# Kernel optimization log

Measured on AMD Instinct MI355X. Metric: run time of the kernel, lower is better.

## Reference

```python
import jax, jax.numpy as jnp
import numpy as np

B, N = 16384, 1024


def _bit_reversal_indices(n):
    bits = int(np.log2(n))
    val = np.arange(n)
    src = np.zeros(n, dtype=np.int64)
    for _ in range(bits):
        src = (src << 1) | (val & 1)
        val = val >> 1
    return src  # src[k] = source pair for target pair k


def _inter_stage_indices(n, stage_idx):
    prev = 2 ** stage_idx
    kb = np.arange(n // 2)
    g = kb // prev
    kw = kb % prev
    half = (kw >= prev // 2).astype(np.int64)
    off = kw % (prev // 2)
    nb = prev // 2
    sE = (2 * g) * nb + off
    sO = (2 * g + 1) * nb + off
    perm = np.empty(n, dtype=np.int64)
    perm[2 * kb] = 2 * sE + half
    perm[2 * kb + 1] = 2 * sO + half
    return perm


def _final_unscramble_indices(n):
    k = np.arange(n // 2)
    perm = np.empty(n, dtype=np.int64)
    perm[k] = 2 * k
    perm[k + n // 2] = 2 * k + 1
    return perm


def _butterfly_weights(n, stage_idx):
    # grouped 1x1 conv weights -> (n//2, 4, 4): out = W[g] @ in per group
    Nb = 2 ** (stage_idx + 1)
    nub = Nb // 2
    reps = n // Nb
    k = np.arange(nub)
    rW = np.cos(2.0 * np.pi * k / Nb)      # Re(W_Nb^k)
    iW = -np.sin(2.0 * np.pi * k / Nb)     # Im(W_Nb^k) (forward DFT twiddle)
    W = np.zeros((nub, 4, 4), dtype=np.float32)
    W[:, 0, 0] = 1.0; W[:, 0, 2] = rW;  W[:, 0, 3] = -iW
    W[:, 1, 1] = 1.0; W[:, 1, 2] = iW;  W[:, 1, 3] = rW
    W[:, 2, 0] = 1.0; W[:, 2, 2] = -rW; W[:, 2, 3] = iW
    W[:, 3, 1] = 1.0; W[:, 3, 2] = -iW; W[:, 3, 3] = -rW
    return np.tile(W, (reps, 1, 1))  # (n//2, 4, 4)


def setup_inputs() -> dict:
    key = jax.random.key(0)
    x = jax.random.normal(key, (B, 2 * N, 1, 1), dtype=jnp.float32)
    return {"x": x}


def reference(x) -> jnp.ndarray:
    b = x.shape[0]
    n = x.shape[1] // 2
    stages = int(np.log2(n))
    # pairs view: (B, N, 2) = interleaved [Re, Im]
    v = x.reshape(b, n, 2)
    v = v[:, jnp.asarray(_bit_reversal_indices(n)), :]
    for s in range(stages):
        if s > 0:
            v = v[:, jnp.asarray(_inter_stage_indices(n, s)), :]
        W = jnp.asarray(_butterfly_weights(n, s))       # (N/2, 4, 4)
        g = v.reshape(b, n // 2, 4)                     # 4 channels per group
        g = jnp.einsum('goi,bgi->bgo', W, g)            # grouped 1x1 conv
        v = g.reshape(b, n, 2)
    v = v[:, jnp.asarray(_final_unscramble_indices(n)), :]
    return v.reshape(b, 2 * n, 1, 1)
```

## Files before the change

### kernel.cpp

```cpp
#include <hip/hip_runtime.h>

#define NFFT 1024

__device__ __forceinline__ float2 cmul(float2 a, float2 b) {
  return make_float2(fmaf(a.x, b.x, -a.y * b.y), fmaf(a.x, b.y, a.y * b.x));
}
__device__ __forceinline__ float2 cadd(float2 a, float2 b) { return make_float2(a.x + b.x, a.y + b.y); }
__device__ __forceinline__ float2 csub(float2 a, float2 b) { return make_float2(a.x - b.x, a.y - b.y); }

__device__ __forceinline__ void dft4(const float2 v[4], float2 y[4]) {
  float2 s02 = cadd(v[0], v[2]), d02 = csub(v[0], v[2]);
  float2 s13 = cadd(v[1], v[3]), d13 = csub(v[1], v[3]);
  y[0] = cadd(s02, s13);
  y[2] = csub(s02, s13);
  y[1] = make_float2(d02.x + d13.y, d02.y - d13.x);
  y[3] = make_float2(d02.x - d13.y, d02.y + d13.x);
}

__device__ __forceinline__ int phys(int s) {
  return (s & ~15) | (((s & 15) + (s >> 4)) & 15);
}

__device__ __forceinline__ void dft16_store(float2 v[16], float2* S, int base, int stride) {
  #pragma unroll
  for (int n2 = 0; n2 < 4; ++n2) {
    float2 a[4] = {v[n2], v[n2 + 4], v[n2 + 8], v[n2 + 12]};
    float2 y[4];
    dft4(a, y);
    v[n2] = y[0]; v[n2 + 4] = y[1]; v[n2 + 8] = y[2]; v[n2 + 12] = y[3];
  }
  const float C1 = 0.9238795325112867f;
  const float S1 = 0.3826834323650898f;
  const float R2 = 0.7071067811865476f;
  v[1 + 4]  = cmul(v[1 + 4],  make_float2(C1, -S1));
  v[1 + 8]  = cmul(v[1 + 8],  make_float2(R2, -R2));
  v[1 + 12] = cmul(v[1 + 12], make_float2(S1, -C1));
  v[2 + 4]  = cmul(v[2 + 4],  make_float2(R2, -R2));
  v[2 + 8]  = make_float2(v[2 + 8].y, -v[2 + 8].x);
  v[2 + 12] = cmul(v[2 + 12], make_float2(-R2, -R2));
  v[3 + 4]  = cmul(v[3 + 4],  make_float2(S1, -C1));
  v[3 + 8]  = cmul(v[3 + 8],  make_float2(-R2, -R2));
  v[3 + 12] = cmul(v[3 + 12], make_float2(-C1, S1));
  #pragma unroll
  for (int k1 = 0; k1 < 4; ++k1) {
    float2 a[4] = {v[4 * k1], v[4 * k1 + 1], v[4 * k1 + 2], v[4 * k1 + 3]};
    float2 y[4];
    dft4(a, y);
    #pragma unroll
    for (int k2 = 0; k2 < 4; ++k2) {
      int k = k1 + 4 * k2;
      S[phys(base + stride * k)] = y[k2];
    }
  }
}

__global__ __launch_bounds__(256) void fft1024_kernel(const float* __restrict__ in,
                                                      float* __restrict__ out) {
  __shared__ float2 lds[4 * NFFT];
  const int wave = threadIdx.x >> 6;
  const int l    = threadIdx.x & 63;
  float2* S = lds + wave * NFFT;
  const int row = blockIdx.x * 4 + wave;
  const float2* xin  = reinterpret_cast<const float2*>(in)  + (size_t)row * NFFT;
  float2*       xout = reinterpret_cast<float2*>(out)       + (size_t)row * NFFT;

  float2 v[16];

  #pragma unroll
  for (int r = 0; r < 16; ++r) v[r] = xin[l + 64 * r];
  dft16_store(v, S, 16 * l, 1);

  #pragma unroll
  for (int r = 0; r < 16; ++r) v[r] = S[phys(l + 64 * r)];
  {
    const float ang = -6.283185307179586f * (float)(l & 15) / 256.0f;
    float sn, cs;
    __sincosf(ang, &sn, &cs);
    const float2 w1 = make_float2(cs, sn);
    float2 w = w1;
    #pragma unroll
    for (int r = 1; r < 16; ++r) {
      v[r] = cmul(v[r], w);
      w = cmul(w, w1);
    }
    const int idxD = ((l >> 4) << 8) | (l & 15);
    dft16_store(v, S, idxD, 16);
  }

  #pragma unroll
  for (int t = 0; t < 4; ++t) {
    const int j = l + 64 * t;
    float2 u[4];
    #pragma unroll
    for (int r = 0; r < 4; ++r) u[r] = S[phys(j + 256 * r)];
    const float ang = -6.283185307179586f * (float)j / 1024.0f;
    float sn, cs;
    __sincosf(ang, &sn, &cs);
    const float2 w1 = make_float2(cs, sn);
    const float2 w2 = cmul(w1, w1);
    const float2 w3 = cmul(w2, w1);
    u[1] = cmul(u[1], w1);
    u[2] = cmul(u[2], w2);
    u[3] = cmul(u[3], w3);
    float2 y[4];
    dft4(u, y);
    #pragma unroll
    for (int r = 0; r < 4; ++r) xout[j + 256 * r] = y[r];
  }
}

extern "C" void kernel_launch(void* const* d_in, const int* in_sizes, int n_in,
                              void* d_out, int out_size, void* d_ws, size_t ws_size,
                              hipStream_t stream) {
  const float* x = (const float*)d_in[0];
  float* out = (float*)d_out;
  const int rows = in_sizes[0] / (2 * NFFT);
  fft1024_kernel<<<rows / 4, 256, 0, stream>>>(x, out);
}
```

Measured before the change: 230.3 us.

## Replace LDS-based FFT passes with register-only wave-shuffle butterflies

Removes the shared-memory scratch and its transposes. Each lane now loads 16 contiguous complex values at a bit-reversed offset and runs a 64-point FFT across lanes with six rounds of __shfl_xor butterflies. It then applies twiddles and finishes with an in-register radix-16 and coalesced stores. The aim is to drop LDS traffic and occupancy limits, and launch bounds request 6 waves per EU. In exchange it issues many cross-lane shuffles (32 per stage), which may cost more than the LDS passes they replace, and loads are strided per lane.

```diff
diff --git a/kernel.cpp b/kernel.cpp
--- a/kernel.cpp
+++ b/kernel.cpp
@@ -17,11 +17,63 @@
   y[3] = make_float2(d02.x - d13.y, d02.y + d13.x);
 }
 
-__device__ __forceinline__ int phys(int s) {
-  return (s & ~15) | (((s & 15) + (s >> 4)) & 15);
-}
+__global__ __launch_bounds__(256, 6) void fft1024_kernel(const float* __restrict__ in,
+                                                         float* __restrict__ out) {
+  const int l = threadIdx.x & 63;
+  const int wave = threadIdx.x >> 6;
+  const int row = blockIdx.x * 4 + wave;
 
-__device__ __forceinline__ void dft16_store(float2 v[16], float2* S, int base, int stride) {
+  const int rb = ((l & 1) << 5) | ((l & 2) << 3) | ((l & 4) << 1) |
+                 ((l & 8) >> 1) | ((l & 16) >> 3) | ((l & 32) >> 5);
+
+  float2 v[16];
+
+  {
+    const float4* in4 = reinterpret_cast<const float4*>(in) + (size_t)row * 512;
+    float4* vf4 = reinterpret_cast<float4*>(v);
+    #pragma unroll
+    for (int o = 0; o < 8; ++o) vf4[o] = in4[8 * rb + o];
+  }
+
+  {
+    float sn, cs;
+    __sincosf(-3.14159265358979323f * (float)(rb & 31) / 32.0f, &sn, &cs);
+    float2 T = make_float2(cs, sn);
+    #pragma unroll
+    for (int s = 0; s < 6; ++s) {
+      const int mask = 1 << s;
+      const bool up = (l & mask) != 0;
+      const float sgn = up ? -1.0f : 1.0f;
+      const float2 tt = up ? T : make_float2(1.0f, 0.0f);
+      #pragma unroll
+      for (int r = 0; r < 16; ++r) {
+        float px = __shfl_xor(v[r].x, mask, 64);
+        float py = __shfl_xor(v[r].y, mask, 64);
+        float ax = fmaf(sgn, v[r].x, px);
+        float ay = fmaf(sgn, v[r].y, py);
+        if (s < 5) v[r] = cmul(make_float2(ax, ay), tt);
+        else       v[r] = make_float2(ax, ay);
+      }
+      if (s < 4) {
+        float2 T2 = cmul(T, T);
+        const float fb = ((rb >> (4 - s)) & 1) ? -1.0f : 1.0f;
+        T = make_float2(T2.x * fb, T2.y * fb);
+      }
+    }
+  }
+
+  {
+    float sn, cs;
+    __sincosf(-6.283185307179586f * (float)l / 1024.0f, &sn, &cs);
+    const float2 u = make_float2(cs, sn);
+    float2 t = u;
+    #pragma unroll
+    for (int r = 1; r < 16; ++r) {
+      v[r] = cmul(v[r], t);
+      if (r < 15) t = cmul(t, u);
+    }
+  }
+
   #pragma unroll
   for (int n2 = 0; n2 < 4; ++n2) {
     float2 a[4] = {v[n2], v[n2 + 4], v[n2 + 8], v[n2 + 12]};
@@ -29,83 +81,32 @@
     dft4(a, y);
     v[n2] = y[0]; v[n2 + 4] = y[1]; v[n2 + 8] = y[2]; v[n2 + 12] = y[3];
   }
-  const float C1 = 0.9238795325112867f;
-  const float S1 = 0.3826834323650898f;
-  const float R2 = 0.7071067811865476f;
-  v[1 + 4]  = cmul(v[1 + 4],  make_float2(C1, -S1));
-  v[1 + 8]  = cmul(v[1 + 8],  make_float2(R2, -R2));
-  v[1 + 12] = cmul(v[1 + 12], make_float2(S1, -C1));
-  v[2 + 4]  = cmul(v[2 + 4],  make_float2(R2, -R2));
-  v[2 + 8]  = make_float2(v[2 + 8].y, -v[2 + 8].x);
-  v[2 + 12] = cmul(v[2 + 12], make_float2(-R2, -R2));
-  v[3 + 4]  = cmul(v[3 + 4],  make_float2(S1, -C1));
-  v[3 + 8]  = cmul(v[3 + 8],  make_float2(-R2, -R2));
-  v[3 + 12] = cmul(v[3 + 12], make_float2(-C1, S1));
-  #pragma unroll
-  for (int k1 = 0; k1 < 4; ++k1) {
-    float2 a[4] = {v[4 * k1], v[4 * k1 + 1], v[4 * k1 + 2], v[4 * k1 + 3]};
-    float2 y[4];
-    dft4(a, y);
+  {
+    const float C1 = 0.9238795325112867f;
+    const float S1 = 0.3826834323650898f;
+    const float R2 = 0.7071067811865476f;
+    v[1 + 4]  = cmul(v[1 + 4],  make_float2(C1, -S1));
+    v[1 + 8]  = cmul(v[1 + 8],  make_float2(R2, -R2));
+    v[1 + 12] = cmul(v[1 + 12], make_float2(S1, -C1));
+    v[2 + 4]  = cmul(v[2 + 4],  make_float2(R2, -R2));
+    v[2 + 8]  = make_float2(v[2 + 8].y, -v[2 + 8].x);
+    v[2 + 12] = cmul(v[2 + 12], make_float2(-R2, -R2));
+    v[3 + 4]  = cmul(v[3 + 4],  make_float2(S1, -C1));
+    v[3 + 8]  = cmul(v[3 + 8],  make_float2(-R2, -R2));
+    v[3 + 12] = cmul(v[3 + 12], make_float2(-C1, S1));
+  }
+  {
+    float2* out2 = reinterpret_cast<float2*>(out) + (size_t)row * NFFT;
     #pragma unroll
-    for (int k2 = 0; k2 < 4; ++k2) {
-      int k = k1 + 4 * k2;
-      S[phys(base + stride * k)] = y[k2];
+    for (int k1 = 0; k1 < 4; ++k1) {
+      float2 a[4] = {v[4 * k1], v[4 * k1 + 1], v[4 * k1 + 2], v[4 * k1 + 3]};
+      float2 y[4];
+      dft4(a, y);
+      #pragma unroll
+      for (int k2 = 0; k2 < 4; ++k2) {
+        out2[l + 64 * (k1 + 4 * k2)] = y[k2];
+      }
     }
-  }
-}
-
-__global__ __launch_bounds__(256) void fft1024_kernel(const float* __restrict__ in,
-                                                      float* __restrict__ out) {
-  __shared__ float2 lds[4 * NFFT];
-  const int wave = threadIdx.x >> 6;
-  const int l    = threadIdx.x & 63;
-  float2* S = lds + wave * NFFT;
-  const int row = blockIdx.x * 4 + wave;
-  const float2* xin  = reinterpret_cast<const float2*>(in)  + (size_t)row * NFFT;
-  float2*       xout = reinterpret_cast<float2*>(out)       + (size_t)row * NFFT;
-
-  float2 v[16];
-
-  #pragma unroll
-  for (int r = 0; r < 16; ++r) v[r] = xin[l + 64 * r];
-  dft16_store(v, S, 16 * l, 1);
-
-  #pragma unroll
-  for (int r = 0; r < 16; ++r) v[r] = S[phys(l + 64 * r)];
-  {
-    const float ang = -6.283185307179586f * (float)(l & 15) / 256.0f;
-    float sn, cs;
-    __sincosf(ang, &sn, &cs);
-    const float2 w1 = make_float2(cs, sn);
-    float2 w = w1;
-    #pragma unroll
-    for (int r = 1; r < 16; ++r) {
-      v[r] = cmul(v[r], w);
-      w = cmul(w, w1);
-    }
-    const int idxD = ((l >> 4) << 8) | (l & 15);
-    dft16_store(v, S, idxD, 16);
-  }
-
-  #pragma unroll
-  for (int t = 0; t < 4; ++t) {
-    const int j = l + 64 * t;
-    float2 u[4];
-    #pragma unroll
-    for (int r = 0; r < 4; ++r) u[r] = S[phys(j + 256 * r)];
-    const float ang = -6.283185307179586f * (float)j / 1024.0f;
-    float sn, cs;
-    __sincosf(ang, &sn, &cs);
-    const float2 w1 = make_float2(cs, sn);
-    const float2 w2 = cmul(w1, w1);
-    const float2 w3 = cmul(w2, w1);
-    u[1] = cmul(u[1], w1);
-    u[2] = cmul(u[2], w2);
-    u[3] = cmul(u[3], w3);
-    float2 y[4];
-    dft4(u, y);
-    #pragma unroll
-    for (int r = 0; r < 4; ++r) xout[j + 256 * r] = y[r];
   }
 }
 
```

Measured after the change: 232.8 us. About the same (+1.1%).
